# Optimization experiments

Measured on AMD Instinct MI355X. Metric: run time of the kernel, lower is better.

Reference implementation:

```python
import jax, jax.numpy as jnp
import numpy as np

DIM = 1024
HEADS = 16
DIM_HEAD = 64
INNER = HEADS * DIM_HEAD  # 1024
MAX_POS = 512
B, N = 2, 1024


def setup_inputs() -> dict:
    key = jax.random.key(0)
    ks = jax.random.split(key, 6)
    s = DIM ** -0.5
    x = jax.random.normal(ks[0], (B, N, DIM), dtype=jnp.float32)
    Wq = jax.random.normal(ks[1], (DIM, INNER), dtype=jnp.float32) * s
    Wkv = jax.random.normal(ks[2], (DIM, 2 * INNER), dtype=jnp.float32) * s
    Wo = jax.random.normal(ks[3], (INNER, DIM), dtype=jnp.float32) * (INNER ** -0.5)
    bo = jnp.zeros((DIM,), dtype=jnp.float32)
    rel_emb = jax.random.normal(ks[4], (2 * MAX_POS + 1, DIM_HEAD), dtype=jnp.float32)
    return {"x": x, "Wq": Wq, "Wkv": Wkv, "Wo": Wo, "bo": bo, "rel_emb": rel_emb}


def reference(x, Wq, Wkv, Wo, bo, rel_emb):
    b, n, _ = x.shape
    scale = DIM_HEAD ** -0.5
    q = x @ Wq                    # [b, n, inner]
    kv = x @ Wkv                  # [b, n, 2*inner]
    k, v = jnp.split(kv, 2, axis=-1)

    def split_heads(t):
        return t.reshape(b, n, HEADS, DIM_HEAD).transpose(0, 2, 1, 3)  # [b,h,n,d]

    q, k, v = map(split_heads, (q, k, v))
    dots = jnp.einsum('bhid,bhjd->bhij', q, k) * scale

    seq = jnp.arange(n)
    dist = jnp.clip(seq[:, None] - seq[None, :], -MAX_POS, MAX_POS) + MAX_POS  # [n, n]
    rel = rel_emb[dist]           # [n, n, d]
    pos_attn = jnp.einsum('bhnd,nrd->bhnr', q, rel) * scale
    dots = dots + pos_attn

    attn = jax.nn.softmax(dots, axis=-1)
    out = jnp.einsum('bhij,bhjd->bhid', attn, v)
    out = out.transpose(0, 2, 1, 3).reshape(b, n, INNER)
    return out @ Wo + bo
```

## Files before the change

kernel.cpp:

```cpp
#include <hip/hip_runtime.h>

typedef __bf16 bf16x8 __attribute__((ext_vector_type(8)));
typedef float f32x4 __attribute__((ext_vector_type(4)));

#define DEV __device__ __forceinline__

DEV unsigned short f2bf(float f) {
  union { float f; unsigned u; } x; x.f = f;
  unsigned r = x.u + 0x7FFFu + ((x.u >> 16) & 1u);
  return (unsigned short)(r >> 16);
}
DEV float bf2f(unsigned short h) {
  union { unsigned u; float f; } x; x.u = ((unsigned)h) << 16;
  return x.f;
}
DEV unsigned short bfc(float f) {
  union { __bf16 b; unsigned short u; } c; c.b = (__bf16)f; return c.u;
}

typedef __attribute__((address_space(3))) void* lds_vp;
typedef const __attribute__((address_space(1))) void* gbl_vp;
DEV void load_lds16(const unsigned short* gp, void* lp) {
  __builtin_amdgcn_global_load_lds((gbl_vp)(const void*)gp, (lds_vp)lp, 16, 0, 0);
}

__global__ __launch_bounds__(256)
void prep_k(const float* __restrict__ x, const float* __restrict__ rel,
            const float* __restrict__ bo, const float* __restrict__ Wq,
            const float* __restrict__ Wkv, const float* __restrict__ Wo,
            unsigned short* __restrict__ xb, unsigned short* __restrict__ relb,
            unsigned short* __restrict__ bob, unsigned short* __restrict__ WqkvT,
            unsigned short* __restrict__ WoT) {
  __shared__ unsigned short tile[32][33];
  const int bid = blockIdx.x, tid = threadIdx.x;
  if (bid < 2114) {
    const float* src; unsigned short* dst; long base; long n;
    if (bid < 2048)      { src = x;   dst = xb;   base = (long)bid * 1024;          n = 2097152; }
    else if (bid < 2113) { src = rel; dst = relb; base = (long)(bid - 2048) * 1024; n = 65600; }
    else                 { src = bo;  dst = bob;  base = 0;                          n = 1024; }
    long i = base + tid * 4;
    if (i < n) {
      float4 v = *(const float4*)&src[i];
      unsigned long long u = (unsigned long long)f2bf(v.x)
                           | ((unsigned long long)f2bf(v.y) << 16)
                           | ((unsigned long long)f2bf(v.z) << 32)
                           | ((unsigned long long)f2bf(v.w) << 48);
      *(unsigned long long*)&dst[i] = u;
    }
  } else {
    int id = bid - 2114;
    const float* src; unsigned short* dst; const int R = 1024; int C, txt, tyt;
    if (id < 1024)      { src = Wq;  dst = WqkvT;           C = 1024; txt = id & 31; tyt = id >> 5; }
    else if (id < 3072) { int l = id - 1024; src = Wkv; dst = WqkvT + 1048576; C = 2048; txt = l & 63; tyt = l >> 6; }
    else                { int l = id - 3072; src = Wo;  dst = WoT;             C = 1024; txt = l & 31; tyt = l >> 5; }
    int c0 = txt * 32, r0 = tyt * 32;
    int tx = tid & 31, ty = tid >> 5;
    #pragma unroll
    for (int i = 0; i < 4; ++i)
      tile[ty + i * 8][tx] = f2bf(src[(size_t)(r0 + ty + i * 8) * C + c0 + tx]);
    __syncthreads();
    #pragma unroll
    for (int i = 0; i < 4; ++i)
      dst[(size_t)(c0 + ty + i * 8) * R + r0 + tx] = tile[tx][ty + i * 8];
  }
}

__global__ __launch_bounds__(256)
void gemm_qkv(const unsigned short* __restrict__ A,
              const unsigned short* __restrict__ Bt,
              unsigned short* __restrict__ o0,
              unsigned short* __restrict__ o1,
              unsigned short* __restrict__ o2) {
  __shared__ __align__(16) unsigned short As[64][32];
  __shared__ __align__(16) unsigned short Bs[128][32];
  __shared__ unsigned short tbuf[64][68];
  const int tid  = threadIdx.x;
  const int lane = tid & 63, wave = tid >> 6;
  const int q15  = lane & 15, quad = lane >> 4;
  const int wr = wave >> 1, wc = wave & 1;
  const int m0 = blockIdx.y * 64, n0 = blockIdx.x * 128;
  const int K = 1024;
  const int lrow = lane >> 2, lkc = (lane & 3) * 8;

  f32x4 acc[2][4] = {};
  for (int k0 = 0; k0 < K; k0 += 32) {
    __syncthreads();
    load_lds16(&A[(size_t)(m0 + wave * 16 + lrow) * K + k0 + lkc], &As[wave * 16][0]);
    #pragma unroll
    for (int t = 0; t < 2; ++t)
      load_lds16(&Bt[(size_t)(n0 + wave * 32 + t * 16 + lrow) * K + k0 + lkc],
                 &Bs[wave * 32 + t * 16][0]);
    __syncthreads();
    bf16x8 af[2], bfr[4];
    #pragma unroll
    for (int i = 0; i < 2; ++i)
      af[i] = *(const bf16x8*)&As[wr * 32 + i * 16 + q15][quad * 8];
    #pragma unroll
    for (int j = 0; j < 4; ++j)
      bfr[j] = *(const bf16x8*)&Bs[wc * 64 + j * 16 + q15][quad * 8];
    #pragma unroll
    for (int i = 0; i < 2; ++i)
      #pragma unroll
      for (int j = 0; j < 4; ++j)
        acc[i][j] = __builtin_amdgcn_mfma_f32_16x16x32_bf16(af[i], bfr[j], acc[i][j], 0, 0, 0);
  }

  const int b = m0 >> 10, nn0 = m0 & 1023;
  if (n0 < 2048) {
    #pragma unroll
    for (int i = 0; i < 2; ++i)
      #pragma unroll
      for (int j = 0; j < 4; ++j)
        #pragma unroll
        for (int r = 0; r < 4; ++r) {
          int row = m0 + wr * 32 + i * 16 + quad * 4 + r;
          int col = n0 + wc * 64 + j * 16 + q15;
          float v = acc[i][j][r];
          int nn = row & 1023;
          unsigned short* dst; int c = col; float sc = 1.f;
          if (col < 1024) { dst = o0; sc = 0.125f; }
          else            { dst = o1; c = col - 1024; }
          int h = c >> 6, dd = c & 63;
          dst[((size_t)((row >> 10) * 16 + h) * 1024 + nn) * 64 + dd] = f2bf(v * sc);
        }
  } else {
    const int hp = (n0 - 2048) >> 6;
    #pragma unroll
    for (int hh = 0; hh < 2; ++hh) {
      __syncthreads();
      if (wc == hh) {
        #pragma unroll
        for (int i = 0; i < 2; ++i)
          #pragma unroll
          for (int j = 0; j < 4; ++j)
            #pragma unroll
            for (int r = 0; r < 4; ++r)
              tbuf[wr * 32 + i * 16 + quad * 4 + r][j * 16 + q15] = f2bf(acc[i][j][r]);
      }
      __syncthreads();
      const int bh = b * 16 + hp + hh;
      const int d = tid >> 2, nb = (tid & 3) * 16;
      #pragma unroll
      for (int s = 0; s < 2; ++s) {
        int n = nb + s * 8;
        union { uint4 v; unsigned short us[8]; } t;
        #pragma unroll
        for (int e = 0; e < 8; ++e) t.us[e] = tbuf[n + e][d];
        *(uint4*)&o2[((size_t)bh * 64 + d) * 1024 + nn0 + n] = t.v;
      }
    }
  }
}

DEV void stage16(const unsigned short* gbase, size_t gstride,
                 unsigned short* lbase, int r0, int lane) {
  #pragma unroll
  for (int t = 0; t < 2; ++t) {
    int r = r0 + t * 8 + (lane >> 3);
    int lc = (lane & 7) ^ (r & 7);
    load_lds16(&gbase[(size_t)r * gstride + lc * 8], &lbase[(size_t)(r0 + t * 8) * 64]);
  }
}
DEV bf16x8 read_swz(const unsigned short* buf, int row, int lc) {
  int pc = lc ^ (row & 7);
  return *(const bf16x8*)&buf[row * 64 + pc * 8];
}

__global__ __launch_bounds__(256)
void flash_attn(const unsigned short* __restrict__ q_ws,
                const unsigned short* __restrict__ k_ws,
                const unsigned short* __restrict__ vt_ws,
                const unsigned short* __restrict__ rel,
                unsigned short* __restrict__ ao) {
  __shared__ __align__(16) unsigned short Kbuf[2][64 * 64];
  __shared__ __align__(16) unsigned short Vbuf[2][64 * 64];
  __shared__ __align__(16) unsigned short P_lds[4][16 * 64];
  __shared__ __align__(16) float T_lds[4][16][84];

  const int tid  = threadIdx.x;
  const int lane = tid & 63, w = tid >> 6;
  const int q15  = lane & 15, quad = lane >> 4;
  const int bh = blockIdx.x;
  const int ib = blockIdx.y * 64 + w * 16;

  const unsigned short* qp = q_ws  + (size_t)bh * 1024 * 64;
  const unsigned short* kp = k_ws  + (size_t)bh * 1024 * 64;
  const unsigned short* tp = vt_ws + (size_t)bh * 64 * 1024;

  bf16x8 aq[2];
  #pragma unroll
  for (int ks = 0; ks < 2; ++ks)
    aq[ks] = *(const bf16x8*)&qp[(size_t)(ib + q15) * 64 + ks * 32 + quad * 8];

  f32x4 o[4] = {};
  float l_i[4] = {0.f, 0.f, 0.f, 0.f};

  stage16(kp, 64, &Kbuf[0][0], w * 16, lane);
  stage16(tp, 1024, &Vbuf[0][0], w * 16, lane);

  for (int jt = 0; jt < 16; ++jt) {
    const int j0 = jt * 64, cur = jt & 1;
    __syncthreads();
    if (jt + 1 < 16) {
      stage16(kp + (size_t)(j0 + 64) * 64, 64, &Kbuf[cur ^ 1][0], w * 16, lane);
      stage16(tp + (j0 + 64), 1024, &Vbuf[cur ^ 1][0], w * 16, lane);
    }

    f32x4 accS[4] = {};
    #pragma unroll
    for (int ks = 0; ks < 2; ++ks)
      #pragma unroll
      for (int cb = 0; cb < 4; ++cb) {
        bf16x8 bk = read_swz(&Kbuf[cur][0], cb * 16 + q15, ks * 4 + quad);
        accS[cb] = __builtin_amdgcn_mfma_f32_16x16x32_bf16(aq[ks], bk, accS[cb], 0, 0, 0);
      }
    int tb = ib - j0 + 512 - 63;
    f32x4 accT[5] = {};
    #pragma unroll
    for (int ks = 0; ks < 2; ++ks)
      #pragma unroll
      for (int ub = 0; ub < 5; ++ub) {
        int trow = tb + ub * 16 + q15;
        trow = trow < 0 ? 0 : (trow > 1024 ? 1024 : trow);
        bf16x8 br = *(const bf16x8*)&rel[(size_t)trow * 64 + ks * 32 + quad * 8];
        accT[ub] = __builtin_amdgcn_mfma_f32_16x16x32_bf16(aq[ks], br, accT[ub], 0, 0, 0);
      }
    #pragma unroll
    for (int ub = 0; ub < 5; ++ub)
      #pragma unroll
      for (int r = 0; r < 4; ++r)
        T_lds[w][quad * 4 + r][ub * 16 + q15] = accT[ub][r];

    #pragma unroll
    for (int r = 0; r < 4; ++r) {
      const int dl = quad * 4 + r;
      #pragma unroll
      for (int cb = 0; cb < 4; ++cb) {
        int dj = cb * 16 + q15;
        float s = accS[cb][r] + T_lds[w][dl][63 + dl - dj];
        float p = exp2f(fmaf(s, 1.44269504f, -64.f));
        l_i[r] += p;
        P_lds[w][dl * 64 + ((((dj >> 3) ^ (dl & 7)) << 3) | (dj & 7))] = bfc(p);
      }
    }

    #pragma unroll
    for (int ks = 0; ks < 2; ++ks) {
      bf16x8 ap = *(const bf16x8*)&P_lds[w][q15 * 64 + (((ks * 4 + quad) ^ (q15 & 7)) << 3)];
      #pragma unroll
      for (int db = 0; db < 4; ++db) {
        bf16x8 bv = read_swz(&Vbuf[cur][0], db * 16 + q15, ks * 4 + quad);
        o[db] = __builtin_amdgcn_mfma_f32_16x16x32_bf16(ap, bv, o[db], 0, 0, 0);
      }
    }
  }

  #pragma unroll
  for (int r = 0; r < 4; ++r) {
    #pragma unroll
    for (int off = 1; off < 16; off <<= 1)
      l_i[r] += __shfl_xor(l_i[r], off, 64);
    l_i[r] = 1.f / (l_i[r] + 1e-30f);
  }

  const int b = bh >> 4, h = bh & 15;
  #pragma unroll
  for (int db = 0; db < 4; ++db)
    #pragma unroll
    for (int r = 0; r < 4; ++r) {
      int row = ib + quad * 4 + r;
      ao[((size_t)(b * 1024 + row)) * 1024 + h * 64 + db * 16 + q15] =
          bfc(o[db][r] * l_i[r]);
    }
}

__global__ __launch_bounds__(256)
void gemm_out(const unsigned short* __restrict__ A,
              const unsigned short* __restrict__ Bt,
              const unsigned short* __restrict__ bias,
              float* __restrict__ fo) {
  __shared__ __align__(16) unsigned short As[64][32];
  __shared__ __align__(16) unsigned short Bs[64][32];
  const int tid  = threadIdx.x;
  const int lane = tid & 63, w = tid >> 6;
  const int q15  = lane & 15, quad = lane >> 4;
  const int m0 = blockIdx.y * 64, n0 = blockIdx.x * 64;
  const int K = 1024, N = 1024;
  const int lrow = lane >> 2, lkc = (lane & 3) * 8;

  f32x4 acc[4] = {};
  for (int k0 = 0; k0 < K; k0 += 32) {
    __syncthreads();
    load_lds16(&A[(size_t)(m0 + w * 16 + lrow) * K + k0 + lkc], &As[w * 16][0]);
    load_lds16(&Bt[(size_t)(n0 + w * 16 + lrow) * K + k0 + lkc], &Bs[w * 16][0]);
    __syncthreads();
    bf16x8 af = *(const bf16x8*)&As[w * 16 + q15][quad * 8];
    bf16x8 bfr[4];
    #pragma unroll
    for (int j = 0; j < 4; ++j)
      bfr[j] = *(const bf16x8*)&Bs[j * 16 + q15][quad * 8];
    #pragma unroll
    for (int j = 0; j < 4; ++j)
      acc[j] = __builtin_amdgcn_mfma_f32_16x16x32_bf16(af, bfr[j], acc[j], 0, 0, 0);
  }
  #pragma unroll
  for (int j = 0; j < 4; ++j)
    #pragma unroll
    for (int r = 0; r < 4; ++r) {
      int row = m0 + w * 16 + quad * 4 + r;
      int col = n0 + j * 16 + q15;
      fo[(size_t)row * N + col] = acc[j][r] + bf2f(bias[col]);
    }
}

extern "C" void kernel_launch(void* const* d_in, const int* in_sizes, int n_in,
                              void* d_out, int out_size, void* d_ws, size_t ws_size,
                              hipStream_t stream) {
  (void)in_sizes; (void)n_in; (void)out_size; (void)ws_size;
  const float* x   = (const float*)d_in[0];
  const float* Wq  = (const float*)d_in[1];
  const float* Wkv = (const float*)d_in[2];
  const float* Wo  = (const float*)d_in[3];
  const float* bo  = (const float*)d_in[4];
  const float* rel = (const float*)d_in[5];
  float* out = (float*)d_out;

  unsigned short* ws = (unsigned short*)d_ws;
  unsigned short* WoT   = ws;
  unsigned short* relb  = WoT   + 1048576;
  unsigned short* bob   = relb  + 65664;
  unsigned short* q_ws  = bob   + 1088;
  unsigned short* k_ws  = q_ws  + 2097152;
  unsigned short* vT    = k_ws  + 2097152;
  unsigned short* WqkvT = vT    + 2097152;
  unsigned short* xb    = WqkvT + 3145728;
  unsigned short* ao    = WqkvT;

  prep_k<<<6210, 256, 0, stream>>>(x, rel, bo, Wq, Wkv, Wo,
                                   xb, relb, bob, WqkvT, WoT);
  gemm_qkv<<<dim3(24, 32), 256, 0, stream>>>(xb, WqkvT, q_ws, k_ws, vT);
  flash_attn<<<dim3(32, 16), 256, 0, stream>>>(q_ws, k_ws, vT, relb, ao);
  gemm_out<<<dim3(16, 32), 256, 0, stream>>>(ao, WoT, bob, out);
}
```

Before: 170.8 us.

## Load K/V straight into registers in attention; deepen GEMM K-tiles with swizzled LDS

The attention kernel drops its shared-memory K/V double buffer and block barriers. Each wave now loads its K and transposed-V fragments directly from global memory into registers, prefetching one tile ahead with two register sets. The QKV and output GEMMs move from 32-wide to 64-wide K tiles, staged with XOR-swizzled LDS so there are half as many barrier pairs. In exchange, the four waves in a block load the same K/V data redundantly from global memory or cache, register pressure rises, and GEMM LDS usage doubles.

```diff
diff --git a/kernel.cpp b/kernel.cpp
--- a/kernel.cpp
+++ b/kernel.cpp
@@ -65,14 +65,28 @@
   }
 }
 
+DEV void stage16(const unsigned short* gbase, size_t gstride,
+                 unsigned short* lbase, int r0, int lane) {
+  #pragma unroll
+  for (int t = 0; t < 2; ++t) {
+    int r = r0 + t * 8 + (lane >> 3);
+    int lc = (lane & 7) ^ (r & 7);
+    load_lds16(&gbase[(size_t)r * gstride + lc * 8], &lbase[(size_t)(r0 + t * 8) * 64]);
+  }
+}
+DEV bf16x8 read_swz(const unsigned short* buf, int row, int lc) {
+  int pc = lc ^ (row & 7);
+  return *(const bf16x8*)&buf[row * 64 + pc * 8];
+}
+
 __global__ __launch_bounds__(256)
 void gemm_qkv(const unsigned short* __restrict__ A,
               const unsigned short* __restrict__ Bt,
               unsigned short* __restrict__ o0,
               unsigned short* __restrict__ o1,
               unsigned short* __restrict__ o2) {
-  __shared__ __align__(16) unsigned short As[64][32];
-  __shared__ __align__(16) unsigned short Bs[128][32];
+  __shared__ __align__(16) unsigned short As[64 * 64];
+  __shared__ __align__(16) unsigned short Bs[128 * 64];
   __shared__ unsigned short tbuf[64][68];
   const int tid  = threadIdx.x;
   const int lane = tid & 63, wave = tid >> 6;
@@ -80,29 +94,29 @@
   const int wr = wave >> 1, wc = wave & 1;
   const int m0 = blockIdx.y * 64, n0 = blockIdx.x * 128;
   const int K = 1024;
-  const int lrow = lane >> 2, lkc = (lane & 3) * 8;
 
   f32x4 acc[2][4] = {};
-  for (int k0 = 0; k0 < K; k0 += 32) {
-    __syncthreads();
-    load_lds16(&A[(size_t)(m0 + wave * 16 + lrow) * K + k0 + lkc], &As[wave * 16][0]);
-    #pragma unroll
-    for (int t = 0; t < 2; ++t)
-      load_lds16(&Bt[(size_t)(n0 + wave * 32 + t * 16 + lrow) * K + k0 + lkc],
-                 &Bs[wave * 32 + t * 16][0]);
-    __syncthreads();
-    bf16x8 af[2], bfr[4];
-    #pragma unroll
-    for (int i = 0; i < 2; ++i)
-      af[i] = *(const bf16x8*)&As[wr * 32 + i * 16 + q15][quad * 8];
-    #pragma unroll
-    for (int j = 0; j < 4; ++j)
-      bfr[j] = *(const bf16x8*)&Bs[wc * 64 + j * 16 + q15][quad * 8];
-    #pragma unroll
-    for (int i = 0; i < 2; ++i)
+  for (int k0 = 0; k0 < K; k0 += 64) {
+    __syncthreads();
+    stage16(&A[(size_t)m0 * K + k0], K, As, wave * 16, lane);
+    stage16(&Bt[(size_t)n0 * K + k0], K, Bs, wave * 32, lane);
+    stage16(&Bt[(size_t)n0 * K + k0], K, Bs, wave * 32 + 16, lane);
+    __syncthreads();
+    #pragma unroll
+    for (int ks = 0; ks < 2; ++ks) {
+      bf16x8 af[2], bfr[4];
+      #pragma unroll
+      for (int i = 0; i < 2; ++i)
+        af[i] = read_swz(As, wr * 32 + i * 16 + q15, ks * 4 + quad);
       #pragma unroll
       for (int j = 0; j < 4; ++j)
-        acc[i][j] = __builtin_amdgcn_mfma_f32_16x16x32_bf16(af[i], bfr[j], acc[i][j], 0, 0, 0);
+        bfr[j] = read_swz(Bs, wc * 64 + j * 16 + q15, ks * 4 + quad);
+      #pragma unroll
+      for (int i = 0; i < 2; ++i)
+        #pragma unroll
+        for (int j = 0; j < 4; ++j)
+          acc[i][j] = __builtin_amdgcn_mfma_f32_16x16x32_bf16(af[i], bfr[j], acc[i][j], 0, 0, 0);
+    }
   }
 
   const int b = m0 >> 10, nn0 = m0 & 1023;
@@ -152,18 +166,66 @@
   }
 }
 
-DEV void stage16(const unsigned short* gbase, size_t gstride,
-                 unsigned short* lbase, int r0, int lane) {
-  #pragma unroll
-  for (int t = 0; t < 2; ++t) {
-    int r = r0 + t * 8 + (lane >> 3);
-    int lc = (lane & 7) ^ (r & 7);
-    load_lds16(&gbase[(size_t)r * gstride + lc * 8], &lbase[(size_t)(r0 + t * 8) * 64]);
-  }
-}
-DEV bf16x8 read_swz(const unsigned short* buf, int row, int lc) {
-  int pc = lc ^ (row & 7);
-  return *(const bf16x8*)&buf[row * 64 + pc * 8];
+DEV void loadKV(const unsigned short* kp, const unsigned short* tp, int j0,
+                int q15, int quad, bf16x8 bk[2][4], bf16x8 bv[2][4]) {
+  #pragma unroll
+  for (int ks = 0; ks < 2; ++ks)
+    #pragma unroll
+    for (int c = 0; c < 4; ++c) {
+      bk[ks][c] = *(const bf16x8*)&kp[(size_t)(j0 + c * 16 + q15) * 64 + ks * 32 + quad * 8];
+      bv[ks][c] = *(const bf16x8*)&tp[(size_t)(c * 16 + q15) * 1024 + j0 + ks * 32 + quad * 8];
+    }
+}
+
+DEV void fstep(int j0, int ib, int q15, int quad,
+               const bf16x8 aq[2], const bf16x8 bk[2][4], const bf16x8 bv[2][4],
+               const unsigned short* __restrict__ rel,
+               float (*T)[84], unsigned short* P,
+               f32x4 o[4], float l_i[4]) {
+  f32x4 accS[4] = {};
+  #pragma unroll
+  for (int ks = 0; ks < 2; ++ks)
+    #pragma unroll
+    for (int cb = 0; cb < 4; ++cb)
+      accS[cb] = __builtin_amdgcn_mfma_f32_16x16x32_bf16(aq[ks], bk[ks][cb], accS[cb], 0, 0, 0);
+
+  int tb = ib - j0 + 512 - 63;
+  f32x4 accT[5] = {};
+  #pragma unroll
+  for (int ks = 0; ks < 2; ++ks)
+    #pragma unroll
+    for (int ub = 0; ub < 5; ++ub) {
+      int trow = tb + ub * 16 + q15;
+      trow = trow < 0 ? 0 : (trow > 1024 ? 1024 : trow);
+      bf16x8 br = *(const bf16x8*)&rel[(size_t)trow * 64 + ks * 32 + quad * 8];
+      accT[ub] = __builtin_amdgcn_mfma_f32_16x16x32_bf16(aq[ks], br, accT[ub], 0, 0, 0);
+    }
+  #pragma unroll
+  for (int ub = 0; ub < 5; ++ub)
+    #pragma unroll
+    for (int r = 0; r < 4; ++r)
+      T[quad * 4 + r][ub * 16 + q15] = accT[ub][r];
+
+  #pragma unroll
+  for (int r = 0; r < 4; ++r) {
+    const int dl = quad * 4 + r;
+    #pragma unroll
+    for (int cb = 0; cb < 4; ++cb) {
+      int dj = cb * 16 + q15;
+      float s = accS[cb][r] + T[dl][63 + dl - dj];
+      float p = exp2f(fmaf(s, 1.44269504f, -64.f));
+      l_i[r] += p;
+      P[dl * 64 + ((((dj >> 3) ^ (dl & 7)) << 3) | (dj & 7))] = bfc(p);
+    }
+  }
+
+  #pragma unroll
+  for (int ks = 0; ks < 2; ++ks) {
+    bf16x8 ap = *(const bf16x8*)&P[q15 * 64 + (((ks * 4 + quad) ^ (q15 & 7)) << 3)];
+    #pragma unroll
+    for (int db = 0; db < 4; ++db)
+      o[db] = __builtin_amdgcn_mfma_f32_16x16x32_bf16(ap, bv[ks][db], o[db], 0, 0, 0);
+  }
 }
 
 __global__ __launch_bounds__(256)
@@ -172,8 +234,6 @@
                 const unsigned short* __restrict__ vt_ws,
                 const unsigned short* __restrict__ rel,
                 unsigned short* __restrict__ ao) {
-  __shared__ __align__(16) unsigned short Kbuf[2][64 * 64];
-  __shared__ __align__(16) unsigned short Vbuf[2][64 * 64];
   __shared__ __align__(16) unsigned short P_lds[4][16 * 64];
   __shared__ __align__(16) float T_lds[4][16][84];
 
@@ -195,64 +255,15 @@
   f32x4 o[4] = {};
   float l_i[4] = {0.f, 0.f, 0.f, 0.f};
 
-  stage16(kp, 64, &Kbuf[0][0], w * 16, lane);
-  stage16(tp, 1024, &Vbuf[0][0], w * 16, lane);
-
-  for (int jt = 0; jt < 16; ++jt) {
-    const int j0 = jt * 64, cur = jt & 1;
-    __syncthreads();
-    if (jt + 1 < 16) {
-      stage16(kp + (size_t)(j0 + 64) * 64, 64, &Kbuf[cur ^ 1][0], w * 16, lane);
-      stage16(tp + (j0 + 64), 1024, &Vbuf[cur ^ 1][0], w * 16, lane);
-    }
-
-    f32x4 accS[4] = {};
-    #pragma unroll
-    for (int ks = 0; ks < 2; ++ks)
-      #pragma unroll
-      for (int cb = 0; cb < 4; ++cb) {
-        bf16x8 bk = read_swz(&Kbuf[cur][0], cb * 16 + q15, ks * 4 + quad);
-        accS[cb] = __builtin_amdgcn_mfma_f32_16x16x32_bf16(aq[ks], bk, accS[cb], 0, 0, 0);
-      }
-    int tb = ib - j0 + 512 - 63;
-    f32x4 accT[5] = {};
-    #pragma unroll
-    for (int ks = 0; ks < 2; ++ks)
-      #pragma unroll
-      for (int ub = 0; ub < 5; ++ub) {
-        int trow = tb + ub * 16 + q15;
-        trow = trow < 0 ? 0 : (trow > 1024 ? 1024 : trow);
-        bf16x8 br = *(const bf16x8*)&rel[(size_t)trow * 64 + ks * 32 + quad * 8];
-        accT[ub] = __builtin_amdgcn_mfma_f32_16x16x32_bf16(aq[ks], br, accT[ub], 0, 0, 0);
-      }
-    #pragma unroll
-    for (int ub = 0; ub < 5; ++ub)
-      #pragma unroll
-      for (int r = 0; r < 4; ++r)
-        T_lds[w][quad * 4 + r][ub * 16 + q15] = accT[ub][r];
-
-    #pragma unroll
-    for (int r = 0; r < 4; ++r) {
-      const int dl = quad * 4 + r;
-      #pragma unroll
-      for (int cb = 0; cb < 4; ++cb) {
-        int dj = cb * 16 + q15;
-        float s = accS[cb][r] + T_lds[w][dl][63 + dl - dj];
-        float p = exp2f(fmaf(s, 1.44269504f, -64.f));
-        l_i[r] += p;
-        P_lds[w][dl * 64 + ((((dj >> 3) ^ (dl & 7)) << 3) | (dj & 7))] = bfc(p);
-      }
-    }
-
-    #pragma unroll
-    for (int ks = 0; ks < 2; ++ks) {
-      bf16x8 ap = *(const bf16x8*)&P_lds[w][q15 * 64 + (((ks * 4 + quad) ^ (q15 & 7)) << 3)];
-      #pragma unroll
-      for (int db = 0; db < 4; ++db) {
-        bf16x8 bv = read_swz(&Vbuf[cur][0], db * 16 + q15, ks * 4 + quad);
-        o[db] = __builtin_amdgcn_mfma_f32_16x16x32_bf16(ap, bv, o[db], 0, 0, 0);
-      }
-    }
+  bf16x8 bkA[2][4], bvA[2][4], bkB[2][4], bvB[2][4];
+  loadKV(kp, tp, 0, q15, quad, bkA, bvA);
+
+  for (int jt = 0; jt < 16; jt += 2) {
+    loadKV(kp, tp, (jt + 1) * 64, q15, quad, bkB, bvB);
+    fstep(jt * 64, ib, q15, quad, aq, bkA, bvA, rel, T_lds[w], P_lds[w], o, l_i);
+    if (jt + 2 < 16)
+      loadKV(kp, tp, (jt + 2) * 64, q15, quad, bkA, bvA);
+    fstep((jt + 1) * 64, ib, q15, quad, aq, bkB, bvB, rel, T_lds[w], P_lds[w], o, l_i);
   }
 
   #pragma unroll
@@ -279,29 +290,31 @@
               const unsigned short* __restrict__ Bt,
               const unsigned short* __restrict__ bias,
               float* __restrict__ fo) {
-  __shared__ __align__(16) unsigned short As[64][32];
-  __shared__ __align__(16) unsigned short Bs[64][32];
+  __shared__ __align__(16) unsigned short As[64 * 64];
+  __shared__ __align__(16) unsigned short Bs[64 * 64];
   const int tid  = threadIdx.x;
   const int lane = tid & 63, w = tid >> 6;
   const int q15  = lane & 15, quad = lane >> 4;
   const int m0 = blockIdx.y * 64, n0 = blockIdx.x * 64;
   const int K = 1024, N = 1024;
-  const int lrow = lane >> 2, lkc = (lane & 3) * 8;
 
   f32x4 acc[4] = {};
-  for (int k0 = 0; k0 < K; k0 += 32) {
-    __syncthreads();
-    load_lds16(&A[(size_t)(m0 + w * 16 + lrow) * K + k0 + lkc], &As[w * 16][0]);
-    load_lds16(&Bt[(size_t)(n0 + w * 16 + lrow) * K + k0 + lkc], &Bs[w * 16][0]);
-    __syncthreads();
-    bf16x8 af = *(const bf16x8*)&As[w * 16 + q15][quad * 8];
-    bf16x8 bfr[4];
-    #pragma unroll
-    for (int j = 0; j < 4; ++j)
-      bfr[j] = *(const bf16x8*)&Bs[j * 16 + q15][quad * 8];
-    #pragma unroll
-    for (int j = 0; j < 4; ++j)
-      acc[j] = __builtin_amdgcn_mfma_f32_16x16x32_bf16(af, bfr[j], acc[j], 0, 0, 0);
+  for (int k0 = 0; k0 < K; k0 += 64) {
+    __syncthreads();
+    stage16(&A[(size_t)m0 * K + k0], K, As, w * 16, lane);
+    stage16(&Bt[(size_t)n0 * K + k0], K, Bs, w * 16, lane);
+    __syncthreads();
+    #pragma unroll
+    for (int ks = 0; ks < 2; ++ks) {
+      bf16x8 af = read_swz(As, w * 16 + q15, ks * 4 + quad);
+      bf16x8 bfr[4];
+      #pragma unroll
+      for (int j = 0; j < 4; ++j)
+        bfr[j] = read_swz(Bs, j * 16 + q15, ks * 4 + quad);
+      #pragma unroll
+      for (int j = 0; j < 4; ++j)
+        acc[j] = __builtin_amdgcn_mfma_f32_16x16x32_bf16(af, bfr[j], acc[j], 0, 0, 0);
+    }
   }
   #pragma unroll
   for (int j = 0; j < 4; ++j)
```

After: 208.4 us. +22.0%, slower.
